# Kernel optimization log

Measured on AMD Instinct MI355X. Metric: run time of the kernel, lower is better.

The kernel has to match this reference:

```python
import jax, jax.numpy as jnp
import numpy as np

N_NODES = 100000
N_EDGES = 1600000
IN_DIM = 160
HID = 128
BN_EPS = 1e-5


def setup_inputs() -> dict:
    key = jax.random.key(0)
    ks = jax.random.split(key, 16)
    d = {}
    d['x'] = jax.random.normal(ks[0], (N_NODES, IN_DIM), dtype=jnp.float32)
    d['edge_index'] = jax.random.randint(ks[1], (2, N_EDGES), 0, N_NODES, dtype=jnp.int64)
    dims = [(IN_DIM, HID), (HID, HID), (HID, HID)]
    for i, (fi, fo) in enumerate(dims):
        s = 1.0 / np.sqrt(fi)
        d[f'wl{i}'] = jax.random.normal(ks[2 + 4 * i], (fi, fo), dtype=jnp.float32) * s
        d[f'wr{i}'] = jax.random.normal(ks[3 + 4 * i], (fi, fo), dtype=jnp.float32) * s
        d[f'bl{i}'] = jnp.zeros((fo,), dtype=jnp.float32)
        d[f'g{i}'] = jnp.ones((fo,), dtype=jnp.float32)
        d[f'be{i}'] = jnp.zeros((fo,), dtype=jnp.float32)
        d[f'rm{i}'] = jax.random.normal(ks[4 + 4 * i], (fo,), dtype=jnp.float32) * 0.1
        d[f'rv{i}'] = jnp.ones((fo,), dtype=jnp.float32)
    d['lin_w'] = jax.random.normal(ks[14], (HID, 1), dtype=jnp.float32) * (1.0 / np.sqrt(HID))
    d['lin_b'] = jnp.zeros((1,), dtype=jnp.float32)
    return d


def _sage_bn_relu(h, src, dst, wl, wr, bl, g, be, rm, rv):
    # mean neighbor aggregation: gather messages at src, scatter-mean to dst
    msg = h[src]                                            # [E, d]
    agg = jax.ops.segment_sum(msg, dst, num_segments=N_NODES)
    cnt = jax.ops.segment_sum(jnp.ones((msg.shape[0],), h.dtype), dst, num_segments=N_NODES)
    mean = agg / jnp.maximum(cnt, 1.0)[:, None]             # nodes w/o in-edges -> 0
    out = mean @ wl + bl + h @ wr                           # SAGEConv (root_weight=True)
    # BatchNorm1d (inference: running stats) + ReLU
    out = (out - rm) * (g * jax.lax.rsqrt(rv + BN_EPS)) + be
    return jax.nn.relu(out)


def reference(x, edge_index,
              wl0, wr0, bl0, g0, be0, rm0, rv0,
              wl1, wr1, bl1, g1, be1, rm1, rv1,
              wl2, wr2, bl2, g2, be2, rm2, rv2,
              lin_w, lin_b):
    src, dst = edge_index[0], edge_index[1]
    h = _sage_bn_relu(x, src, dst, wl0, wr0, bl0, g0, be0, rm0, rv0)
    h = _sage_bn_relu(h, src, dst, wl1, wr1, bl1, g1, be1, rm1, rv1)
    h = _sage_bn_relu(h, src, dst, wl2, wr2, bl2, g2, be2, rm2, rv2)
    return (h @ lin_w + lin_b)[:, 0]                        # [N]
```

## Files before the change

### kernel.cpp

```cpp
#include <hip/hip_runtime.h>

#define N_NODES 100000
#define N_EDGES 1600000
#define IN_DIM 160
#define HID 128
#define BN_EPS 1e-5f

#define M_PAD 100096
#define NBUCK 196
#define BSH 9
#define EPB 8192
#define NHB (NBUCK * NBUCK)
#define LPAD 132

typedef unsigned int uint;
typedef unsigned short ushort;
typedef __attribute__((ext_vector_type(8))) short bf16x8;
typedef __attribute__((ext_vector_type(4))) float f32x4;
typedef __attribute__((ext_vector_type(2))) float f32x2;

__device__ __forceinline__ ushort bf16rn(float f) {
    uint u = __float_as_uint(f);
    u += 0x7fffu + ((u >> 16) & 1u);
    return (ushort)(u >> 16);
}
__device__ __forceinline__ float bflo(uint u) { return __uint_as_float(u << 16); }
__device__ __forceinline__ float bfhi(uint u) { return __uint_as_float(u & 0xffff0000u); }


__device__ __forceinline__ void prep_body(int ob, int lane, const float* __restrict__ wl,
                                          const float* __restrict__ wr,
                                          ushort* __restrict__ Bf, int K) {
    int kb = ob >> 4;
    int tt = ob & 15;
    int n = tt * 16 + (lane & 15);
    int k0 = kb * 32 + (lane >> 4) * 8;
    ushort* dst = Bf + ((size_t)(kb * 16 + tt) * 64 + lane) * 8;
#pragma unroll
    for (int e = 0; e < 8; ++e) {
        int k = k0 + e;
        float v = (n < HID) ? wl[k * HID + n] : wr[k * HID + (n - HID)];
        dst[e] = bf16rn(v);
    }
}

#define PREP0_B 20
#define PREP1_B 16
#define INIT_GRID (NBUCK + PREP0_B + 2 * PREP1_B + 2)

__global__ __launch_bounds__(256) void init_kernel(
    const int* __restrict__ dst, int* __restrict__ ghist,
    const float* __restrict__ wl0, const float* __restrict__ wr0,
    const float* __restrict__ wl1, const float* __restrict__ wr1,
    const float* __restrict__ wl2, const float* __restrict__ wr2,
    ushort* __restrict__ Bf0, ushort* __restrict__ Bf1, ushort* __restrict__ Bf2,
    const float* __restrict__ bl0, const float* __restrict__ g0,
    const float* __restrict__ be0, const float* __restrict__ rm0,
    const float* __restrict__ rv0,
    const float* __restrict__ bl1, const float* __restrict__ g1,
    const float* __restrict__ be1, const float* __restrict__ rm1,
    const float* __restrict__ rv1,
    const float* __restrict__ bl2, const float* __restrict__ g2,
    const float* __restrict__ be2, const float* __restrict__ rm2,
    const float* __restrict__ rv2,
    float* __restrict__ bnscale, float* __restrict__ bnshift) {
    __shared__ int hist[NBUCK];
    int b = blockIdx.x, t = threadIdx.x;
    if (b < NBUCK) {
        for (int i = t; i < NBUCK; i += 256) hist[i] = 0;
        __syncthreads();
        int e0 = b * EPB;
        for (int i = 0; i < EPB; i += 256) {
            int e = e0 + i + t;
            if (e < N_EDGES) atomicAdd(&hist[dst[e] >> BSH], 1);
        }
        __syncthreads();
        for (int i = t; i < NBUCK; i += 256) ghist[i * NBUCK + b] = hist[i];
    } else if (b < NBUCK + PREP0_B) {
        prep_body((b - NBUCK) * 4 + (t >> 6), t & 63, wl0, wr0, Bf0, IN_DIM);
    } else if (b < NBUCK + PREP0_B + PREP1_B) {
        prep_body((b - NBUCK - PREP0_B) * 4 + (t >> 6), t & 63, wl1, wr1, Bf1, HID);
    } else if (b < NBUCK + PREP0_B + 2 * PREP1_B) {
        prep_body((b - NBUCK - PREP0_B - PREP1_B) * 4 + (t >> 6), t & 63, wl2, wr2, Bf2, HID);
    } else {
        int tt = (b - (NBUCK + PREP0_B + 2 * PREP1_B)) * 256 + t;
        if (tt < 3 * HID) {
            int L = tt >> 7, j = tt & 127;
            const float* bl = (L == 0) ? bl0 : (L == 1) ? bl1 : bl2;
            const float* gg = (L == 0) ? g0  : (L == 1) ? g1  : g2;
            const float* be = (L == 0) ? be0 : (L == 1) ? be1 : be2;
            const float* rm = (L == 0) ? rm0 : (L == 1) ? rm1 : rm2;
            const float* rv = (L == 0) ? rv0 : (L == 1) ? rv1 : rv2;
            float s = gg[j] * rsqrtf(rv[j] + BN_EPS);
            bnscale[tt] = s;
            bnshift[tt] = (bl[j] - rm[j]) * s + be[j];
        }
    }
}

#define SPT 38

__global__ __launch_bounds__(1024) void scan_all_kernel(int* __restrict__ ghist,
                                                        int* __restrict__ gbb) {
    __shared__ int ts[1024];
    int t = threadIdx.x;
    int base = t * SPT;
    int v[SPT];
    int s = 0;
#pragma unroll
    for (int i = 0; i < SPT; ++i) {
        int idx = base + i;
        int x = (idx < NHB) ? ghist[idx] : 0;
        v[i] = s;
        s += x;
    }
    ts[t] = s;
    __syncthreads();
    for (int off = 1; off < 1024; off <<= 1) {
        int a = (t >= off) ? ts[t - off] : 0;
        __syncthreads();
        ts[t] += a;
        __syncthreads();
    }
    int ex = (t > 0) ? ts[t - 1] : 0;
#pragma unroll
    for (int i = 0; i < SPT; ++i) {
        int idx = base + i;
        if (idx < NHB) {
            int e = ex + v[i];
            ghist[idx] = e;
            if (idx % NBUCK == 0) gbb[idx / NBUCK] = e;
        }
    }
    if (t == 0) gbb[NBUCK] = N_EDGES;
}


__global__ __launch_bounds__(256) void bucket_csr_kernel(const uint* __restrict__ scat,
                                                         const int* __restrict__ gbb,
                                                         int* __restrict__ prow,
                                                         int* __restrict__ deg,
                                                         int* __restrict__ peidx) {
    __shared__ int cnt[512], fl[512], pref[512];
    __shared__ int ts[256];
    __shared__ int tot_s;
    int b = blockIdx.x, t = threadIdx.x;
    int beg = gbb[b], end = gbb[b + 1];
    int pb = beg + b * 8192;
    cnt[t] = 0; cnt[t + 256] = 0;
    __syncthreads();
    for (int i = beg + t; i < end; i += 256)
        atomicAdd(&cnt[scat[i] >> 17], 1);
    __syncthreads();
    int c0 = cnt[2 * t], c1 = cnt[2 * t + 1];
    int p0 = (c0 + 15) & ~15, p1 = (c1 + 15) & ~15;
    ts[t] = p0 + p1;
    __syncthreads();
    for (int off = 1; off < 256; off <<= 1) {
        int v = (t >= off) ? ts[t - off] : 0;
        __syncthreads();
        ts[t] += v;
        __syncthreads();
    }
    int ex = (t > 0) ? ts[t - 1] : 0;
    pref[2 * t] = ex;
    pref[2 * t + 1] = ex + p0;
    fl[t] = 0; fl[t + 256] = 0;
    if (t == 255) tot_s = ts[255];
    int g0 = b * 512 + 2 * t;
    if (g0 < N_NODES) { prow[g0] = pb + ex; deg[g0] = c0; }
    if (g0 + 1 < N_NODES) { prow[g0 + 1] = pb + ex + p0; deg[g0 + 1] = c1; }
    __syncthreads();
    int tot = tot_s;
    for (int i = t; i < tot; i += 256) peidx[pb + i] = N_NODES;
    __syncthreads();
    for (int i = beg + t; i < end; i += 256) {
        uint w = scat[i];
        int nl = (int)(w >> 17);
        int lp = atomicAdd(&fl[nl], 1);
        peidx[pb + pref[nl] + lp] = (int)(w & 0x1FFFFu);
    }
}

template <int K, bool AFP32>
__device__ __forceinline__ void gemm_body(int bx, int t, ushort* ldsA,
                                          const void* __restrict__ A_,
                                          const ushort* __restrict__ Bf,
                                          ushort* __restrict__ tl,
                                          ushort* __restrict__ troot) {
    constexpr int CPR = K / 8;
    constexpr int FULLG = CPR & ~7;
    const int m0b = bx * 64;

#pragma unroll
    for (int i = 0; i < (64 * CPR) / 256; ++i) {
        int cidx = i * 256 + t;
        int row = cidx / CPR;
        int j = cidx - row * CPR;
        bf16x8 v;
        if (AFP32) {
            const float* A = (const float*)A_;
            int m = m0b + row;
            float4 f0 = make_float4(0.f, 0.f, 0.f, 0.f), f1 = f0;
            if (m < N_NODES) {
                f0 = *(const float4*)(A + (size_t)m * K + j * 8);
                f1 = *(const float4*)(A + (size_t)m * K + j * 8 + 4);
            }
            v[0] = (short)bf16rn(f0.x); v[1] = (short)bf16rn(f0.y);
            v[2] = (short)bf16rn(f0.z); v[3] = (short)bf16rn(f0.w);
            v[4] = (short)bf16rn(f1.x); v[5] = (short)bf16rn(f1.y);
            v[6] = (short)bf16rn(f1.z); v[7] = (short)bf16rn(f1.w);
        } else {
            const ushort* A = (const ushort*)A_;
            v = *(const bf16x8*)(A + (size_t)(m0b + row) * K + j * 8);
        }
        int swz = (j < FULLG) ? ((j & ~7) | ((j ^ row) & 7))
                              : ((j & ~3) | ((j ^ row) & 3));
        *(bf16x8*)&ldsA[row * K + swz * 8] = v;
    }
    __syncthreads();

    const int lane = t & 63;
    const int wv = t >> 6;
    const int col = lane & 15;
    const int q = lane >> 4;
    const int rh = wv & 1;
    const int ch = wv >> 1;
    const int row0 = rh * 32 + col;
    f32x4 acc0[8], acc1[8];
#pragma unroll
    for (int tt = 0; tt < 8; ++tt) {
        acc0[tt] = (f32x4){0.f, 0.f, 0.f, 0.f};
        acc1[tt] = (f32x4){0.f, 0.f, 0.f, 0.f};
    }

#pragma unroll
    for (int kb = 0; kb < K / 32; ++kb) {
        int jj = kb * 4 + q;
        int swzj = (jj < FULLG) ? ((jj & ~7) | ((jj ^ col) & 7))
                                : ((jj & ~3) | ((jj ^ col) & 3));
        bf16x8 a0 = *(const bf16x8*)&ldsA[row0 * K + swzj * 8];
        bf16x8 a1 = *(const bf16x8*)&ldsA[(row0 + 16) * K + swzj * 8];
        const ushort* bp = Bf + ((size_t)((kb * 16 + ch * 8) * 64) + lane) * 8;
#pragma unroll
        for (int tt = 0; tt < 8; ++tt) {
            bf16x8 bfr = *(const bf16x8*)(bp + (size_t)tt * 64 * 8);
            acc0[tt] = __builtin_amdgcn_mfma_f32_16x16x32_bf16(a0, bfr, acc0[tt], 0, 0, 0);
            acc1[tt] = __builtin_amdgcn_mfma_f32_16x16x32_bf16(a1, bfr, acc1[tt], 0, 0, 0);
        }
    }

    __syncthreads();
    ushort(*rp)[16][LPAD] = (ushort(*)[16][LPAD])ldsA;
    ushort* outp = ch ? troot : tl;
#pragma unroll
    for (int mt = 0; mt < 2; ++mt) {
        const f32x4* ac = mt ? acc1 : acc0;
#pragma unroll
        for (int tt = 0; tt < 8; ++tt)
#pragma unroll
            for (int r = 0; r < 4; ++r)
                rp[wv][q * 4 + r][tt * 16 + col] = bf16rn(ac[tt][r]);
        int mbase = m0b + rh * 32 + mt * 16;
#pragma unroll
        for (int i = 0; i < 4; ++i) {
            int lin = i * 64 + lane;
            int row = lin >> 4;
            int c16 = lin & 15;
            bf16x8 v = *(const bf16x8*)&rp[wv][row][c16 * 8];
            *(bf16x8*)(outp + (size_t)(mbase + row) * HID + c16 * 8) = v;
        }
    }
}

__global__ __launch_bounds__(256) void scatter_gemm1_kernel(
    const int* __restrict__ src, const int* __restrict__ dst,
    const int* __restrict__ ghist, uint* __restrict__ scat,
    const float* __restrict__ x, const ushort* __restrict__ Bf0,
    ushort* __restrict__ tl, ushort* __restrict__ troot) {
    constexpr int LDSE = (64 * IN_DIM > 4 * 16 * LPAD) ? 64 * IN_DIM : 4 * 16 * LPAD;
    __shared__ ushort ldsA[LDSE];
    int b = blockIdx.x, t = threadIdx.x;
    if (b < NBUCK) {
        int* base = (int*)ldsA;
        int* fill = base + NBUCK;
        for (int i = t; i < NBUCK; i += 256) { base[i] = ghist[i * NBUCK + b]; fill[i] = 0; }
        __syncthreads();
        int e0 = b * EPB;
        for (int i = 0; i < EPB; i += 256) {
            int e = e0 + i + t;
            if (e < N_EDGES) {
                int d = dst[e];
                int sv = src[e];
                int bk = d >> BSH;
                int lp = atomicAdd(&fill[bk], 1);
                scat[base[bk] + lp] = (uint)sv | ((uint)(d & 511) << 17);
            }
        }
    } else {
        gemm_body<IN_DIM, true>(b - NBUCK, t, ldsA, x, Bf0, tl, troot);
    }
}

__global__ __launch_bounds__(256) void fused_agg_gemm_kernel(
    const ushort* __restrict__ tl_in, const ushort* __restrict__ troot_in,
    const int* __restrict__ prow, const int* __restrict__ deg_,
    const int* __restrict__ peidx,
    const float* __restrict__ bnscale, const float* __restrict__ bnshift,
    const ushort* __restrict__ Bf,
    ushort* __restrict__ tl_out, ushort* __restrict__ troot_out) {
    constexpr int K = HID;
    constexpr int LDSE = (64 * K > 4 * 16 * LPAD) ? 64 * K : 4 * 16 * LPAD;
    __shared__ ushort ldsA[LDSE];
    const int t = threadIdx.x;
    const int lane = t & 63;
    const int wv = t >> 6;
    const int m0b = blockIdx.x * 64;
    const int g = lane >> 4;
    const int s = lane & 15;
    const int gsel = (lane & 48) << 2;

    for (int r = 0; r < 4; ++r) {
        const int row = wv * 16 + r * 4 + g;
        const int n = m0b + row;
        const bool valid = (n < N_NODES);
        const int nn = valid ? n : 0;
        int pbeg = prow[nn];
        int dg = valid ? deg_[nn] : 0;
        int myb = (dg + 15) >> 4;

        f32x2 acc2[4];
#pragma unroll
        for (int i = 0; i < 4; ++i) acc2[i] = (f32x2){0.f, 0.f};

        bool act = (0 < myb);
        int idx = act ? peidx[pbeg + s] : N_NODES;
        int b = 0;
        while (__any(act)) {
            uint4 u[8];
#pragma unroll
            for (int jj = 0; jj < 8; ++jj) {
                int srcj = __builtin_amdgcn_ds_bpermute(gsel | (jj << 2), idx);
                u[jj] = *(const uint4*)(tl_in + (size_t)srcj * HID + s * 8);
            }
#pragma unroll
            for (int jj = 0; jj < 8; ++jj) {
                acc2[0] += (f32x2){bflo(u[jj].x), bfhi(u[jj].x)};
                acc2[1] += (f32x2){bflo(u[jj].y), bfhi(u[jj].y)};
                acc2[2] += (f32x2){bflo(u[jj].z), bfhi(u[jj].z)};
                acc2[3] += (f32x2){bflo(u[jj].w), bfhi(u[jj].w)};
            }
#pragma unroll
            for (int jj = 0; jj < 8; ++jj) {
                int srcj = __builtin_amdgcn_ds_bpermute(gsel | ((jj + 8) << 2), idx);
                u[jj] = *(const uint4*)(tl_in + (size_t)srcj * HID + s * 8);
            }
            ++b;
            bool actn = (b < myb);
            int idxn = actn ? peidx[pbeg + b * 16 + s] : N_NODES;
#pragma unroll
            for (int jj = 0; jj < 8; ++jj) {
                acc2[0] += (f32x2){bflo(u[jj].x), bfhi(u[jj].x)};
                acc2[1] += (f32x2){bflo(u[jj].y), bfhi(u[jj].y)};
                acc2[2] += (f32x2){bflo(u[jj].z), bfhi(u[jj].z)};
                acc2[3] += (f32x2){bflo(u[jj].w), bfhi(u[jj].w)};
            }
            act = actn; idx = idxn;
        }

        float inv = 1.0f / (float)((dg > 0) ? dg : 1);
        uint4 rv = *(const uint4*)(troot_in + (size_t)nn * HID + s * 8);
        float4 sc0 = *(const float4*)(bnscale + s * 8);
        float4 sc1 = *(const float4*)(bnscale + s * 8 + 4);
        float4 sh0 = *(const float4*)(bnshift + s * 8);
        float4 sh1 = *(const float4*)(bnshift + s * 8 + 4);
        float vm = valid ? 1.0f : 0.0f;
        float o[8];
        o[0] = fmaxf(fmaf(fmaf(acc2[0].x, inv, bflo(rv.x)), sc0.x, sh0.x), 0.f) * vm;
        o[1] = fmaxf(fmaf(fmaf(acc2[0].y, inv, bfhi(rv.x)), sc0.y, sh0.y), 0.f) * vm;
        o[2] = fmaxf(fmaf(fmaf(acc2[1].x, inv, bflo(rv.y)), sc0.z, sh0.z), 0.f) * vm;
        o[3] = fmaxf(fmaf(fmaf(acc2[1].y, inv, bfhi(rv.y)), sc0.w, sh0.w), 0.f) * vm;
        o[4] = fmaxf(fmaf(fmaf(acc2[2].x, inv, bflo(rv.z)), sc1.x, sh1.x), 0.f) * vm;
        o[5] = fmaxf(fmaf(fmaf(acc2[2].y, inv, bfhi(rv.z)), sc1.y, sh1.y), 0.f) * vm;
        o[6] = fmaxf(fmaf(fmaf(acc2[3].x, inv, bflo(rv.w)), sc1.z, sh1.z), 0.f) * vm;
        o[7] = fmaxf(fmaf(fmaf(acc2[3].y, inv, bfhi(rv.w)), sc1.w, sh1.w), 0.f) * vm;

        bf16x8 pk;
#pragma unroll
        for (int e = 0; e < 8; ++e) pk[e] = (short)bf16rn(o[e]);
        int swz = (s & ~7) | ((s ^ row) & 7);
        *(bf16x8*)&ldsA[row * K + swz * 8] = pk;
    }
    __syncthreads();

    const int col = lane & 15;
    const int q = lane >> 4;
    const int rh = wv & 1;
    const int ch = wv >> 1;
    const int row0 = rh * 32 + col;
    f32x4 acc0[8], acc1[8];
#pragma unroll
    for (int tt = 0; tt < 8; ++tt) {
        acc0[tt] = (f32x4){0.f, 0.f, 0.f, 0.f};
        acc1[tt] = (f32x4){0.f, 0.f, 0.f, 0.f};
    }
#pragma unroll
    for (int kb = 0; kb < K / 32; ++kb) {
        int jj = kb * 4 + q;
        int swzj = (jj & ~7) | ((jj ^ col) & 7);
        bf16x8 a0 = *(const bf16x8*)&ldsA[row0 * K + swzj * 8];
        bf16x8 a1 = *(const bf16x8*)&ldsA[(row0 + 16) * K + swzj * 8];
        const ushort* bp = Bf + ((size_t)((kb * 16 + ch * 8) * 64) + lane) * 8;
#pragma unroll
        for (int tt = 0; tt < 8; ++tt) {
            bf16x8 bfr = *(const bf16x8*)(bp + (size_t)tt * 64 * 8);
            acc0[tt] = __builtin_amdgcn_mfma_f32_16x16x32_bf16(a0, bfr, acc0[tt], 0, 0, 0);
            acc1[tt] = __builtin_amdgcn_mfma_f32_16x16x32_bf16(a1, bfr, acc1[tt], 0, 0, 0);
        }
    }

    __syncthreads();
    ushort(*rp)[16][LPAD] = (ushort(*)[16][LPAD])ldsA;
    ushort* outp = ch ? troot_out : tl_out;
#pragma unroll
    for (int mt = 0; mt < 2; ++mt) {
        const f32x4* ac = mt ? acc1 : acc0;
#pragma unroll
        for (int tt = 0; tt < 8; ++tt)
#pragma unroll
            for (int rr = 0; rr < 4; ++rr)
                rp[wv][q * 4 + rr][tt * 16 + col] = bf16rn(ac[tt][rr]);
        int mbase = m0b + rh * 32 + mt * 16;
#pragma unroll
        for (int i = 0; i < 4; ++i) {
            int lin = i * 64 + lane;
            int rowi = lin >> 4;
            int c16 = lin & 15;
            bf16x8 v = *(const bf16x8*)&rp[wv][rowi][c16 * 8];
            *(bf16x8*)(outp + (size_t)(mbase + rowi) * HID + c16 * 8) = v;
        }
    }
}

__global__ __launch_bounds__(256) void agg_final_kernel(
    const ushort* __restrict__ tl_, const ushort* __restrict__ troot_,
    const int* __restrict__ prow, const int* __restrict__ deg_,
    const int* __restrict__ peidx,
    const float* __restrict__ bnscale, const float* __restrict__ bnshift,
    const float* __restrict__ linw, const float* __restrict__ linb,
    float* __restrict__ out) {
    const int lane = threadIdx.x & 63;
    const int wvg = (blockIdx.x * 256 + (int)threadIdx.x) >> 6;
    const int g = lane >> 4;
    const int s = lane & 15;
    const int n = wvg * 4 + g;

    int pbeg = prow[n];
    int dg = deg_[n];
    int myb = (dg + 15) >> 4;

    f32x2 acc2[4];
#pragma unroll
    for (int i = 0; i < 4; ++i) acc2[i] = (f32x2){0.f, 0.f};

    const int gsel = (lane & 48) << 2;

    bool act = (0 < myb);
    int idx = act ? peidx[pbeg + s] : N_NODES;
    int b = 0;
    while (__any(act)) {
        uint4 u[16];
#pragma unroll
        for (int jj = 0; jj < 16; ++jj) {
            int srcj = __builtin_amdgcn_ds_bpermute(gsel | (jj << 2), idx);
            u[jj] = *(const uint4*)(tl_ + (size_t)srcj * HID + s * 8);
        }
        ++b;
        bool actn = (b < myb);
        int idxn = actn ? peidx[pbeg + b * 16 + s] : N_NODES;
#pragma unroll
        for (int jj = 0; jj < 16; ++jj) {
            acc2[0] += (f32x2){bflo(u[jj].x), bfhi(u[jj].x)};
            acc2[1] += (f32x2){bflo(u[jj].y), bfhi(u[jj].y)};
            acc2[2] += (f32x2){bflo(u[jj].z), bfhi(u[jj].z)};
            acc2[3] += (f32x2){bflo(u[jj].w), bfhi(u[jj].w)};
        }
        act = actn; idx = idxn;
    }

    float inv = 1.0f / (float)((dg > 0) ? dg : 1);
    uint4 rv = *(const uint4*)(troot_ + (size_t)n * HID + s * 8);
    float4 sc0 = *(const float4*)(bnscale + s * 8);
    float4 sc1 = *(const float4*)(bnscale + s * 8 + 4);
    float4 sh0 = *(const float4*)(bnshift + s * 8);
    float4 sh1 = *(const float4*)(bnshift + s * 8 + 4);
    float o[8];
    o[0] = fmaxf(fmaf(fmaf(acc2[0].x, inv, bflo(rv.x)), sc0.x, sh0.x), 0.f);
    o[1] = fmaxf(fmaf(fmaf(acc2[0].y, inv, bfhi(rv.x)), sc0.y, sh0.y), 0.f);
    o[2] = fmaxf(fmaf(fmaf(acc2[1].x, inv, bflo(rv.y)), sc0.z, sh0.z), 0.f);
    o[3] = fmaxf(fmaf(fmaf(acc2[1].y, inv, bfhi(rv.y)), sc0.w, sh0.w), 0.f);
    o[4] = fmaxf(fmaf(fmaf(acc2[2].x, inv, bflo(rv.z)), sc1.x, sh1.x), 0.f);
    o[5] = fmaxf(fmaf(fmaf(acc2[2].y, inv, bfhi(rv.z)), sc1.y, sh1.y), 0.f);
    o[6] = fmaxf(fmaf(fmaf(acc2[3].x, inv, bflo(rv.w)), sc1.z, sh1.z), 0.f);
    o[7] = fmaxf(fmaf(fmaf(acc2[3].y, inv, bfhi(rv.w)), sc1.w, sh1.w), 0.f);

    float4 w0 = *(const float4*)(linw + s * 8);
    float4 w1 = *(const float4*)(linw + s * 8 + 4);
    float p = o[0] * w0.x + o[1] * w0.y + o[2] * w0.z + o[3] * w0.w +
              o[4] * w1.x + o[5] * w1.y + o[6] * w1.z + o[7] * w1.w;
#pragma unroll
    for (int off = 1; off < 16; off <<= 1) p += __shfl_xor(p, off);
    if (s == 0) out[n] = p + linb[0];
}


extern "C" void kernel_launch(void* const* d_in, const int* in_sizes, int n_in,
                              void* d_out, int out_size, void* d_ws, size_t ws_size,
                              hipStream_t stream) {
    const float* x    = (const float*)d_in[0];
    const int*   ei   = (const int*)d_in[1];
    const int*   esrc = ei;
    const int*   edst = ei + N_EDGES;
    const float* wl[3]; const float* wr[3]; const float* bl[3];
    const float* g[3];  const float* be[3]; const float* rm[3]; const float* rv[3];
    for (int i = 0; i < 3; ++i) {
        wl[i] = (const float*)d_in[2 + 7 * i];
        wr[i] = (const float*)d_in[3 + 7 * i];
        bl[i] = (const float*)d_in[4 + 7 * i];
        g[i]  = (const float*)d_in[5 + 7 * i];
        be[i] = (const float*)d_in[6 + 7 * i];
        rm[i] = (const float*)d_in[7 + 7 * i];
        rv[i] = (const float*)d_in[8 + 7 * i];
    }
    const float* lin_w = (const float*)d_in[23];
    const float* lin_b = (const float*)d_in[24];
    float* out = (float*)d_out;

    char* ws = (char*)d_ws;
    size_t off = 0;
    auto carve = [&](size_t bytes) -> void* {
        void* p = ws + off;
        off += (bytes + 255) & ~(size_t)255;
        return p;
    };
    int*    prow   = (int*)carve((size_t)(N_NODES + 8) * sizeof(int));
    int*    deg    = (int*)carve((size_t)(N_NODES + 8) * sizeof(int));
    int*    peidx  = (int*)carve((size_t)3210000 * sizeof(int));
    uint*   scat   = (uint*)carve((size_t)N_EDGES * sizeof(uint));
    int*    ghist  = (int*)carve((size_t)(NHB + 256) * sizeof(int));
    int*    gbb    = (int*)carve((NBUCK + 4) * sizeof(int));
    ushort* tl0    = (ushort*)carve((size_t)(M_PAD + 1) * HID * sizeof(ushort));
    ushort* troot0 = (ushort*)carve((size_t)M_PAD * HID * sizeof(ushort));
    ushort* tl1    = (ushort*)carve((size_t)(M_PAD + 1) * HID * sizeof(ushort));
    ushort* troot1 = (ushort*)carve((size_t)M_PAD * HID * sizeof(ushort));
    ushort* Bf0    = (ushort*)carve(256 * IN_DIM * sizeof(ushort));
    ushort* Bf1    = (ushort*)carve(256 * HID * sizeof(ushort));
    ushort* Bf2    = (ushort*)carve(256 * HID * sizeof(ushort));
    float*  bnsc   = (float*)carve(3 * HID * sizeof(float));
    float*  bnsh   = (float*)carve(3 * HID * sizeof(float));
    (void)ws_size; (void)n_in; (void)in_sizes; (void)out_size;

    const int GEMM_GRID = M_PAD / 64;
    const int AGGF_GRID = N_NODES / 16;

    init_kernel<<<INIT_GRID, 256, 0, stream>>>(
        edst, ghist,
        wl[0], wr[0], wl[1], wr[1], wl[2], wr[2], Bf0, Bf1, Bf2,
        bl[0], g[0], be[0], rm[0], rv[0],
        bl[1], g[1], be[1], rm[1], rv[1],
        bl[2], g[2], be[2], rm[2], rv[2],
        bnsc, bnsh);
    scan_all_kernel<<<1, 1024, 0, stream>>>(ghist, gbb);
    scatter_gemm1_kernel<<<NBUCK + GEMM_GRID, 256, 0, stream>>>(
        esrc, edst, ghist, scat, x, Bf0, tl0, troot0);
    bucket_csr_kernel<<<NBUCK, 256, 0, stream>>>(scat, gbb, prow, deg, peidx);

    fused_agg_gemm_kernel<<<GEMM_GRID, 256, 0, stream>>>(
        tl0, troot0, prow, deg, peidx, bnsc, bnsh, Bf1, tl1, troot1);
    fused_agg_gemm_kernel<<<GEMM_GRID, 256, 0, stream>>>(
        tl1, troot1, prow, deg, peidx, bnsc + HID, bnsh + HID, Bf2, tl0, troot0);
    agg_final_kernel<<<AGGF_GRID, 256, 0, stream>>>(
        tl0, troot0, prow, deg, peidx, bnsc + 2 * HID, bnsh + 2 * HID,
        lin_w, lin_b, out);
}
```

Baseline: 463.0 us.

## Fold scan into init via last-block, overlap CSR build with first GEMM

```diff
diff --git a/kernel.cpp b/kernel.cpp
--- a/kernel.cpp
+++ b/kernel.cpp
@@ -49,7 +49,8 @@
 #define INIT_GRID (NBUCK + PREP0_B + 2 * PREP1_B + 2)
 
 __global__ __launch_bounds__(256) void init_kernel(
-    const int* __restrict__ dst, int* __restrict__ ghist,
+    const int* __restrict__ dst, int* __restrict__ ghist, int* __restrict__ gbb,
+    int* __restrict__ done_ctr,
     const float* __restrict__ wl0, const float* __restrict__ wr0,
     const float* __restrict__ wl1, const float* __restrict__ wr1,
     const float* __restrict__ wl2, const float* __restrict__ wr2,
@@ -65,6 +66,8 @@
     const float* __restrict__ rv2,
     float* __restrict__ bnscale, float* __restrict__ bnshift) {
     __shared__ int hist[NBUCK];
+    __shared__ int ts2[256];
+    __shared__ int is_last;
     int b = blockIdx.x, t = threadIdx.x;
     if (b < NBUCK) {
         for (int i = t; i < NBUCK; i += 256) hist[i] = 0;
@@ -96,89 +99,68 @@
             bnshift[tt] = (bl[j] - rm[j]) * s + be[j];
         }
     }
-}
-
-#define SPT 38
-
-__global__ __launch_bounds__(1024) void scan_all_kernel(int* __restrict__ ghist,
-                                                        int* __restrict__ gbb) {
-    __shared__ int ts[1024];
-    int t = threadIdx.x;
-    int base = t * SPT;
-    int v[SPT];
+    __threadfence();
+    if (t == 0) is_last = (atomicAdd(done_ctr, 1) == INIT_GRID - 1);
+    __syncthreads();
+    if (!is_last) return;
+    __threadfence();
+    int base4 = t * 38;
     int s = 0;
 #pragma unroll
-    for (int i = 0; i < SPT; ++i) {
-        int idx = base + i;
-        int x = (idx < NHB) ? ghist[idx] : 0;
-        v[i] = s;
-        s += x;
-    }
-    ts[t] = s;
-    __syncthreads();
-    for (int off = 1; off < 1024; off <<= 1) {
-        int a = (t >= off) ? ts[t - off] : 0;
-        __syncthreads();
-        ts[t] += a;
-        __syncthreads();
-    }
-    int ex = (t > 0) ? ts[t - 1] : 0;
-#pragma unroll
-    for (int i = 0; i < SPT; ++i) {
-        int idx = base + i;
-        if (idx < NHB) {
-            int e = ex + v[i];
-            ghist[idx] = e;
-            if (idx % NBUCK == 0) gbb[idx / NBUCK] = e;
+    for (int i = 0; i < 38; ++i) {
+        int i4 = base4 + i;
+        if (i4 * 4 < NHB) {
+            int4 v = ((const int4*)ghist)[i4];
+            s += v.x + v.y + v.z + v.w;
+        }
+    }
+    ts2[t] = s;
+    __syncthreads();
+    for (int off = 1; off < 256; off <<= 1) {
+        int a = (t >= off) ? ts2[t - off] : 0;
+        __syncthreads();
+        ts2[t] += a;
+        __syncthreads();
+    }
+    int run = (t > 0) ? ts2[t - 1] : 0;
+#pragma unroll
+    for (int i = 0; i < 38; ++i) {
+        int i4 = base4 + i;
+        if (i4 * 4 < NHB) {
+            int4 v = ((const int4*)ghist)[i4];
+            int4 w;
+            w.x = run;
+            w.y = w.x + v.x;
+            w.z = w.y + v.y;
+            w.w = w.z + v.z;
+            run = w.w + v.w;
+            ((int4*)ghist)[i4] = w;
+            int idx = i4 * 4;
+            if (idx % NBUCK == 0) gbb[idx / NBUCK] = w.x;
         }
     }
     if (t == 0) gbb[NBUCK] = N_EDGES;
 }
 
-
-__global__ __launch_bounds__(256) void bucket_csr_kernel(const uint* __restrict__ scat,
-                                                         const int* __restrict__ gbb,
-                                                         int* __restrict__ prow,
-                                                         int* __restrict__ deg,
-                                                         int* __restrict__ peidx) {
-    __shared__ int cnt[512], fl[512], pref[512];
-    __shared__ int ts[256];
-    __shared__ int tot_s;
+__global__ __launch_bounds__(256) void scatter_kernel(const int* __restrict__ src,
+                                                      const int* __restrict__ dst,
+                                                      const int* __restrict__ ghist,
+                                                      uint* __restrict__ scat) {
+    __shared__ int base[NBUCK];
+    __shared__ int fill[NBUCK];
     int b = blockIdx.x, t = threadIdx.x;
-    int beg = gbb[b], end = gbb[b + 1];
-    int pb = beg + b * 8192;
-    cnt[t] = 0; cnt[t + 256] = 0;
-    __syncthreads();
-    for (int i = beg + t; i < end; i += 256)
-        atomicAdd(&cnt[scat[i] >> 17], 1);
-    __syncthreads();
-    int c0 = cnt[2 * t], c1 = cnt[2 * t + 1];
-    int p0 = (c0 + 15) & ~15, p1 = (c1 + 15) & ~15;
-    ts[t] = p0 + p1;
-    __syncthreads();
-    for (int off = 1; off < 256; off <<= 1) {
-        int v = (t >= off) ? ts[t - off] : 0;
-        __syncthreads();
-        ts[t] += v;
-        __syncthreads();
-    }
-    int ex = (t > 0) ? ts[t - 1] : 0;
-    pref[2 * t] = ex;
-    pref[2 * t + 1] = ex + p0;
-    fl[t] = 0; fl[t + 256] = 0;
-    if (t == 255) tot_s = ts[255];
-    int g0 = b * 512 + 2 * t;
-    if (g0 < N_NODES) { prow[g0] = pb + ex; deg[g0] = c0; }
-    if (g0 + 1 < N_NODES) { prow[g0 + 1] = pb + ex + p0; deg[g0 + 1] = c1; }
-    __syncthreads();
-    int tot = tot_s;
-    for (int i = t; i < tot; i += 256) peidx[pb + i] = N_NODES;
-    __syncthreads();
-    for (int i = beg + t; i < end; i += 256) {
-        uint w = scat[i];
-        int nl = (int)(w >> 17);
-        int lp = atomicAdd(&fl[nl], 1);
-        peidx[pb + pref[nl] + lp] = (int)(w & 0x1FFFFu);
+    for (int i = t; i < NBUCK; i += 256) { base[i] = ghist[i * NBUCK + b]; fill[i] = 0; }
+    __syncthreads();
+    int e0 = b * EPB;
+    for (int i = 0; i < EPB; i += 256) {
+        int e = e0 + i + t;
+        if (e < N_EDGES) {
+            int d = dst[e];
+            int sv = src[e];
+            int bk = d >> BSH;
+            int lp = atomicAdd(&fill[bk], 1);
+            scat[base[bk] + lp] = (uint)sv | ((uint)(d & 511) << 17);
+        }
     }
 }
 
@@ -273,29 +255,54 @@
     }
 }
 
-__global__ __launch_bounds__(256) void scatter_gemm1_kernel(
-    const int* __restrict__ src, const int* __restrict__ dst,
-    const int* __restrict__ ghist, uint* __restrict__ scat,
+__global__ __launch_bounds__(256) void csr_gemm1_kernel(
+    const uint* __restrict__ scat, const int* __restrict__ gbb,
+    int* __restrict__ prow, int* __restrict__ deg, int* __restrict__ peidx,
     const float* __restrict__ x, const ushort* __restrict__ Bf0,
     ushort* __restrict__ tl, ushort* __restrict__ troot) {
     constexpr int LDSE = (64 * IN_DIM > 4 * 16 * LPAD) ? 64 * IN_DIM : 4 * 16 * LPAD;
     __shared__ ushort ldsA[LDSE];
     int b = blockIdx.x, t = threadIdx.x;
     if (b < NBUCK) {
-        int* base = (int*)ldsA;
-        int* fill = base + NBUCK;
-        for (int i = t; i < NBUCK; i += 256) { base[i] = ghist[i * NBUCK + b]; fill[i] = 0; }
-        __syncthreads();
-        int e0 = b * EPB;
-        for (int i = 0; i < EPB; i += 256) {
-            int e = e0 + i + t;
-            if (e < N_EDGES) {
-                int d = dst[e];
-                int sv = src[e];
-                int bk = d >> BSH;
-                int lp = atomicAdd(&fill[bk], 1);
-                scat[base[bk] + lp] = (uint)sv | ((uint)(d & 511) << 17);
-            }
+        int* cnt  = (int*)ldsA;
+        int* fl   = cnt + 512;
+        int* pref = fl + 512;
+        int* ts   = pref + 512;
+        int* tot_s = ts + 256;
+        int beg = gbb[b], end = gbb[b + 1];
+        int pb = ((beg + 15) & ~15) + b * 8192;
+        cnt[t] = 0; cnt[t + 256] = 0;
+        __syncthreads();
+        for (int i = beg + t; i < end; i += 256)
+            atomicAdd(&cnt[scat[i] >> 17], 1);
+        __syncthreads();
+        int c0 = cnt[2 * t], c1 = cnt[2 * t + 1];
+        int p0 = (c0 + 15) & ~15, p1 = (c1 + 15) & ~15;
+        ts[t] = p0 + p1;
+        __syncthreads();
+        for (int off = 1; off < 256; off <<= 1) {
+            int v = (t >= off) ? ts[t - off] : 0;
+            __syncthreads();
+            ts[t] += v;
+            __syncthreads();
+        }
+        int ex = (t > 0) ? ts[t - 1] : 0;
+        pref[2 * t] = ex;
+        pref[2 * t + 1] = ex + p0;
+        fl[t] = 0; fl[t + 256] = 0;
+        if (t == 255) *tot_s = ts[255];
+        int g0 = b * 512 + 2 * t;
+        if (g0 < N_NODES) { prow[g0] = pb + ex; deg[g0] = c0; }
+        if (g0 + 1 < N_NODES) { prow[g0 + 1] = pb + ex + p0; deg[g0 + 1] = c1; }
+        __syncthreads();
+        int tot = *tot_s;
+        for (int i = t; i < tot; i += 256) peidx[pb + i] = N_NODES;
+        __syncthreads();
+        for (int i = beg + t; i < end; i += 256) {
+            uint w = scat[i];
+            int nl = (int)(w >> 17);
+            int lp = atomicAdd(&fl[nl], 1);
+            peidx[pb + pref[nl] + lp] = (int)(w & 0x1FFFFu);
         }
     } else {
         gemm_body<IN_DIM, true>(b - NBUCK, t, ldsA, x, Bf0, tl, troot);
@@ -320,6 +327,11 @@
     const int s = lane & 15;
     const int gsel = (lane & 48) << 2;
 
+    float4 sc0 = *(const float4*)(bnscale + s * 8);
+    float4 sc1 = *(const float4*)(bnscale + s * 8 + 4);
+    float4 sh0 = *(const float4*)(bnshift + s * 8);
+    float4 sh1 = *(const float4*)(bnshift + s * 8 + 4);
+
     for (int r = 0; r < 4; ++r) {
         const int row = wv * 16 + r * 4 + g;
         const int n = m0b + row;
@@ -337,29 +349,17 @@
         int idx = act ? peidx[pbeg + s] : N_NODES;
         int b = 0;
         while (__any(act)) {
-            uint4 u[8];
-#pragma unroll
-            for (int jj = 0; jj < 8; ++jj) {
+            uint4 u[16];
+#pragma unroll
+            for (int jj = 0; jj < 16; ++jj) {
                 int srcj = __builtin_amdgcn_ds_bpermute(gsel | (jj << 2), idx);
-                u[jj] = *(const uint4*)(tl_in + (size_t)srcj * HID + s * 8);
-            }
-#pragma unroll
-            for (int jj = 0; jj < 8; ++jj) {
-                acc2[0] += (f32x2){bflo(u[jj].x), bfhi(u[jj].x)};
-                acc2[1] += (f32x2){bflo(u[jj].y), bfhi(u[jj].y)};
-                acc2[2] += (f32x2){bflo(u[jj].z), bfhi(u[jj].z)};
-                acc2[3] += (f32x2){bflo(u[jj].w), bfhi(u[jj].w)};
-            }
-#pragma unroll
-            for (int jj = 0; jj < 8; ++jj) {
-                int srcj = __builtin_amdgcn_ds_bpermute(gsel | ((jj + 8) << 2), idx);
                 u[jj] = *(const uint4*)(tl_in + (size_t)srcj * HID + s * 8);
             }
             ++b;
             bool actn = (b < myb);
             int idxn = actn ? peidx[pbeg + b * 16 + s] : N_NODES;
 #pragma unroll
-            for (int jj = 0; jj < 8; ++jj) {
+            for (int jj = 0; jj < 16; ++jj) {
                 acc2[0] += (f32x2){bflo(u[jj].x), bfhi(u[jj].x)};
                 acc2[1] += (f32x2){bflo(u[jj].y), bfhi(u[jj].y)};
                 acc2[2] += (f32x2){bflo(u[jj].z), bfhi(u[jj].z)};
@@ -370,10 +370,6 @@
 
         float inv = 1.0f / (float)((dg > 0) ? dg : 1);
         uint4 rv = *(const uint4*)(troot_in + (size_t)nn * HID + s * 8);
-        float4 sc0 = *(const float4*)(bnscale + s * 8);
-        float4 sc1 = *(const float4*)(bnscale + s * 8 + 4);
-        float4 sh0 = *(const float4*)(bnshift + s * 8);
-        float4 sh1 = *(const float4*)(bnshift + s * 8 + 4);
         float vm = valid ? 1.0f : 0.0f;
         float o[8];
         o[0] = fmaxf(fmaf(fmaf(acc2[0].x, inv, bflo(rv.x)), sc0.x, sh0.x), 0.f) * vm;
@@ -549,10 +545,11 @@
     uint*   scat   = (uint*)carve((size_t)N_EDGES * sizeof(uint));
     int*    ghist  = (int*)carve((size_t)(NHB + 256) * sizeof(int));
     int*    gbb    = (int*)carve((NBUCK + 4) * sizeof(int));
+    int*    done   = (int*)carve(16 * sizeof(int));
     ushort* tl0    = (ushort*)carve((size_t)(M_PAD + 1) * HID * sizeof(ushort));
-    ushort* troot0 = (ushort*)carve((size_t)M_PAD * HID * sizeof(ushort));
+    ushort* troot0 = (ushort*)carve((size_t)(M_PAD + 1) * HID * sizeof(ushort));
     ushort* tl1    = (ushort*)carve((size_t)(M_PAD + 1) * HID * sizeof(ushort));
-    ushort* troot1 = (ushort*)carve((size_t)M_PAD * HID * sizeof(ushort));
+    ushort* troot1 = (ushort*)carve((size_t)(M_PAD + 1) * HID * sizeof(ushort));
     ushort* Bf0    = (ushort*)carve(256 * IN_DIM * sizeof(ushort));
     ushort* Bf1    = (ushort*)carve(256 * HID * sizeof(ushort));
     ushort* Bf2    = (ushort*)carve(256 * HID * sizeof(ushort));
@@ -563,17 +560,18 @@
     const int GEMM_GRID = M_PAD / 64;
     const int AGGF_GRID = N_NODES / 16;
 
+    hipMemsetAsync(done, 0, sizeof(int), stream);
+
     init_kernel<<<INIT_GRID, 256, 0, stream>>>(
-        edst, ghist,
+        edst, ghist, gbb, done,
         wl[0], wr[0], wl[1], wr[1], wl[2], wr[2], Bf0, Bf1, Bf2,
         bl[0], g[0], be[0], rm[0], rv[0],
         bl[1], g[1], be[1], rm[1], rv[1],
         bl[2], g[2], be[2], rm[2], rv[2],
         bnsc, bnsh);
-    scan_all_kernel<<<1, 1024, 0, stream>>>(ghist, gbb);
-    scatter_gemm1_kernel<<<NBUCK + GEMM_GRID, 256, 0, stream>>>(
-        esrc, edst, ghist, scat, x, Bf0, tl0, troot0);
-    bucket_csr_kernel<<<NBUCK, 256, 0, stream>>>(scat, gbb, prow, deg, peidx);
+    scatter_kernel<<<NBUCK, 256, 0, stream>>>(esrc, edst, ghist, scat);
+    csr_gemm1_kernel<<<NBUCK + GEMM_GRID, 256, 0, stream>>>(
+        scat, gbb, prow, deg, peidx, x, Bf0, tl0, troot0);
 
     fused_agg_gemm_kernel<<<GEMM_GRID, 256, 0, stream>>>(
         tl0, troot0, prow, deg, peidx, bnsc, bnsh, Bf1, tl1, troot1);
```

Result: slower. 477.4 us (+3.1%).
